# Performance work log

Measured on AMD Instinct MI355X. Metric: run time of the kernel, lower is better.

## Reference

```python
import jax, jax.numpy as jnp
import numpy as np

NUM_ITER = 5
DIM = 512
BATCH = 64


def setup_inputs() -> dict:
    key = jax.random.key(0)
    a = jax.random.normal(key, (BATCH, DIM, DIM), dtype=jnp.float32)
    # Symmetric PSD input (covariance-like), as in bilinear pooling; Newton-Schulz
    # requires SPD matrices for convergence.
    x = jnp.einsum('bik,bjk->bij', a, a) / DIM
    I = jnp.eye(DIM, dtype=jnp.float32)
    return {"x": x, "I": I}


def reference(x, I):
    # x: [bs, dim, dim]; I: [dim, dim]
    normA = jnp.sqrt(jnp.sum(x * x, axis=(1, 2), keepdims=True))  # Frobenius norm per matrix
    Y = x / normA
    bs, dim, _ = x.shape
    Z = jnp.broadcast_to(I, (bs, dim, dim))
    Ib = Z
    for _ in range(NUM_ITER):
        T = 0.5 * (3.0 * Ib - jnp.matmul(Z, Y))
        Y = jnp.matmul(Y, T)
        Z = jnp.matmul(T, Z)
    sA = Y * jnp.sqrt(normA)
    return sA
```

## Files before the change

kernel.cpp:

```cpp
#include <hip/hip_runtime.h>
#include <hip/hip_bf16.h>
#include <stdint.h>

#define DIM   512
#define BATCH 64
#define KENC  1024
#define BM    256
#define BN    256
#define BKT   32
#define NKT   16
#define BUFE  32768

typedef __attribute__((ext_vector_type(8))) short short8;
typedef __attribute__((ext_vector_type(4))) float floatx4;

__device__ __forceinline__ ushort f2bf(float f) {
    __hip_bfloat16 h = __float2bfloat16(f);
    return *(ushort*)&h;
}
__device__ __forceinline__ float bf2f(ushort u) {
    __hip_bfloat16 h = *(__hip_bfloat16*)&u;
    return (float)h;
}

typedef __attribute__((address_space(3))) uint32_t lds_u32;
typedef const __attribute__((address_space(1))) uint32_t glb_u32;
__device__ __forceinline__ void gload16(const ushort* g, ushort* l) {
    __builtin_amdgcn_global_load_lds((glb_u32*)g, (lds_u32*)l, 16, 0, 0);
}

#define WAITVM(N) asm volatile("s_waitcnt vmcnt(" #N ")" ::: "memory")
#define BARRIER() do { __builtin_amdgcn_s_barrier(); __builtin_amdgcn_sched_barrier(0); } while (0)

__global__ __launch_bounds__(256) void norm_partial_kernel(const float* __restrict__ x,
                                                           float* __restrict__ partial) {
    int b = blockIdx.y;
    int i = blockIdx.x;
    const float4* xv = (const float4*)(x + (size_t)b * DIM * DIM + (size_t)i * (DIM * DIM / 16));
    float s = 0.f;
    #pragma unroll
    for (int r = 0; r < 16; ++r) {
        float4 v = xv[r * 256 + threadIdx.x];
        s += v.x * v.x + v.y * v.y + v.z * v.z + v.w * v.w;
    }
    #pragma unroll
    for (int off = 32; off > 0; off >>= 1) s += __shfl_down(s, off, 64);
    __shared__ float red[4];
    int lane = threadIdx.x & 63, wid = threadIdx.x >> 6;
    if (lane == 0) red[wid] = s;
    __syncthreads();
    if (threadIdx.x == 0) partial[b * 16 + i] = red[0] + red[1] + red[2] + red[3];
}

__global__ __launch_bounds__(256) void init_kernel(const float* __restrict__ x,
                                                   const float* __restrict__ partial,
                                                   float* __restrict__ norms,
                                                   ushort* __restrict__ Yenc,
                                                   ushort* __restrict__ Tenc) {
    int b = blockIdx.y;
    float s = 0.f;
    #pragma unroll
    for (int p = 0; p < 16; ++p) s += partial[b * 16 + p];
    float nrm = sqrtf(s);
    if (blockIdx.x == 0 && threadIdx.x == 0) norms[b] = nrm;
    float inv = 1.0f / nrm;
    int idx = (blockIdx.x * 256 + threadIdx.x) * 4;
    int r = idx >> 9;
    int c = idx & 511;
    float4 v = *(const float4*)(x + (size_t)b * DIM * DIM + idx);
    float yv[4] = {v.x * inv, v.y * inv, v.z * inv, v.w * inv};
    size_t base = (size_t)b * DIM * KENC + (size_t)r * KENC;
    ushort yhi[4], ylo[4], thi[4], tlo[4];
    #pragma unroll
    for (int j = 0; j < 4; ++j) {
        float y = yv[j];
        yhi[j] = f2bf(y);
        ylo[j] = f2bf(y - bf2f(yhi[j]));
        float t = ((c + j) == r ? 1.5f : 0.0f) - 0.5f * y;
        thi[j] = f2bf(t);
        tlo[j] = f2bf(t - bf2f(thi[j]));
    }
    *(ushort4*)(Yenc + base + c)       = *(ushort4*)yhi;
    *(ushort4*)(Yenc + base + 512 + c) = *(ushort4*)ylo;
    *(ushort4*)(Tenc + base + c)       = *(ushort4*)thi;
    *(ushort4*)(Tenc + base + 512 + c) = *(ushort4*)tlo;
}

__device__ __forceinline__ void stage_hi(ushort* buf, const ushort* Ag, const ushort* Bg,
                                         int k0, int tid) {
    #pragma unroll
    for (int s = 0; s < 2; ++s) {
        int vt = tid + s * 512;
        int row = vt >> 2;
        int pc  = vt & 3;
        int kc  = ((pc ^ ((row >> 1) & 3)) << 3);
        const ushort* ar = Ag + (size_t)row * KENC + k0 + kc;
        const ushort* br = Bg + (size_t)row * KENC + k0 + kc;
        gload16(ar, &buf[vt * 8]);
        gload16(br, &buf[16384 + vt * 8]);
    }
}
__device__ __forceinline__ void stage_lo(ushort* buf, const ushort* Ag, const ushort* Bg,
                                         int k0, int tid) {
    #pragma unroll
    for (int s = 0; s < 2; ++s) {
        int vt = tid + s * 512;
        int row = vt >> 2;
        int pc  = vt & 3;
        int kc  = ((pc ^ ((row >> 1) & 3)) << 3);
        const ushort* ar = Ag + (size_t)row * KENC + k0 + kc;
        const ushort* br = Bg + (size_t)row * KENC + k0 + kc;
        gload16(ar + 512, &buf[8192 + vt * 8]);
        gload16(br + 512, &buf[24576 + vt * 8]);
    }
}

__device__ __forceinline__ void store_enc(ushort* Cenc, size_t matoff, int gr, int gc, float v) {
    ushort hi = f2bf(v);
    ushort lo = f2bf(v - bf2f(hi));
    Cenc[matoff + (size_t)gr * KENC + gc] = hi;
    Cenc[matoff + (size_t)gr * KENC + 512 + gc] = lo;
}

template <int MODE>
__global__ __launch_bounds__(512, 2) void gemm_bt(const ushort* __restrict__ A,
                                                  const ushort* __restrict__ B,
                                                  ushort* __restrict__ Cenc,
                                                  float* __restrict__ Cout,
                                                  const float* __restrict__ norms) {
    __shared__ __attribute__((aligned(16))) ushort sm[2 * BUFE];

    int f = blockIdx.x;
    int xcd = f & 7;
    int g   = f >> 3;
    int b   = xcd + 8 * (g >> 2);
    int t   = g & 3;
    int bm  = t >> 1;
    int bn  = t & 1;

    size_t matoff = (size_t)b * DIM * KENC;
    const ushort* Ag = A + matoff + (size_t)bm * BM * KENC;
    const ushort* Bg = B + matoff + (size_t)bn * BN * KENC;

    int tid = threadIdx.x;
    int wave = tid >> 6, lane = tid & 63;
    int lane15 = lane & 15, quad = lane >> 4;
    int wrow = (wave >> 2) * 128;
    int wcol = (wave & 3) * 64;
    int s2 = (lane15 >> 1) & 3;
    int fo = ((quad ^ s2) << 3);

    floatx4 acc[8][4];
    #pragma unroll
    for (int i = 0; i < 8; ++i)
        #pragma unroll
        for (int j = 0; j < 4; ++j)
            acc[i][j] = (floatx4){0.f, 0.f, 0.f, 0.f};

    stage_hi(sm, Ag, Bg, 0, tid);
    stage_lo(sm, Ag, Bg, 0, tid);
    WAITVM(4);
    BARRIER();

    short8 ah[8], bh[4], bl[4], al[8];
    #pragma unroll
    for (int i = 0; i < 8; ++i)
        ah[i] = *(const short8*)&sm[(wrow + i * 16 + lane15) * BKT + fo];
    #pragma unroll
    for (int j = 0; j < 4; ++j)
        bh[j] = *(const short8*)&sm[16384 + (wcol + j * 16 + lane15) * BKT + fo];

    for (int kt = 0; kt < NKT; ++kt) {
        const ushort* cur = sm + (kt & 1) * BUFE;
        ushort* nxt = sm + ((kt + 1) & 1) * BUFE;
        const ushort* Asl = cur + 8192;
        const ushort* Bsl = cur + 24576;

        if (kt + 1 < NKT) stage_hi(nxt, Ag, Bg, (kt + 1) * BKT, tid);
        __builtin_amdgcn_s_setprio(1);
        #pragma unroll
        for (int i = 0; i < 8; ++i)
            #pragma unroll
            for (int j = 0; j < 4; ++j)
                acc[i][j] = __builtin_amdgcn_mfma_f32_16x16x32_bf16(ah[i], bh[j], acc[i][j], 0, 0, 0);
        __builtin_amdgcn_s_setprio(0);

        if (kt + 1 < NKT) { WAITVM(4); } else { WAITVM(0); }
        BARRIER();

        #pragma unroll
        for (int j = 0; j < 4; ++j)
            bl[j] = *(const short8*)&Bsl[(wcol + j * 16 + lane15) * BKT + fo];
        #pragma unroll
        for (int i = 0; i < 8; ++i)
            al[i] = *(const short8*)&Asl[(wrow + i * 16 + lane15) * BKT + fo];
        if (kt + 1 < NKT) stage_lo(nxt, Ag, Bg, (kt + 1) * BKT, tid);
        __builtin_amdgcn_s_setprio(1);
        #pragma unroll
        for (int i = 0; i < 8; ++i)
            #pragma unroll
            for (int j = 0; j < 4; ++j)
                acc[i][j] = __builtin_amdgcn_mfma_f32_16x16x32_bf16(ah[i], bl[j], acc[i][j], 0, 0, 0);
        #pragma unroll
        for (int i = 0; i < 8; ++i)
            #pragma unroll
            for (int j = 0; j < 4; ++j)
                acc[i][j] = __builtin_amdgcn_mfma_f32_16x16x32_bf16(al[i], bh[j], acc[i][j], 0, 0, 0);
        __builtin_amdgcn_s_setprio(0);

        if (kt + 1 < NKT) {
            WAITVM(4);
            BARRIER();
            #pragma unroll
            for (int i = 0; i < 8; ++i)
                ah[i] = *(const short8*)&nxt[(wrow + i * 16 + lane15) * BKT + fo];
            #pragma unroll
            for (int j = 0; j < 4; ++j)
                bh[j] = *(const short8*)&nxt[16384 + (wcol + j * 16 + lane15) * BKT + fo];
        }
    }

    float scale = (MODE == 2) ? sqrtf(norms[b]) : 0.f;
    #pragma unroll
    for (int i = 0; i < 8; ++i) {
        int gr0 = bm * BM + wrow + i * 16 + quad * 4;
        #pragma unroll
        for (int j = 0; j < 4; ++j) {
            int gc = bn * BN + wcol + j * 16 + lane15;
            #pragma unroll
            for (int rr = 0; rr < 4; ++rr) {
                int gr = gr0 + rr;
                float cv = acc[i][j][rr];
                if (MODE == 0) {
                    store_enc(Cenc, matoff, gr, gc, (gr == gc ? 1.5f : 0.0f) - 0.5f * cv);
                } else if (MODE == 1) {
                    store_enc(Cenc, matoff, gr, gc, cv);
                } else {
                    Cout[(size_t)b * DIM * DIM + (size_t)gr * DIM + gc] = cv * scale;
                }
            }
        }
    }
}

extern "C" void kernel_launch(void* const* d_in, const int* in_sizes, int n_in,
                              void* d_out, int out_size, void* d_ws, size_t ws_size,
                              hipStream_t stream) {
    const float* x = (const float*)d_in[0];
    float* out = (float*)d_out;

    const size_t MATB = (size_t)BATCH * DIM * KENC * sizeof(ushort);
    char* ws = (char*)d_ws;
    ushort* W0 = (ushort*)(ws + 0 * MATB);
    ushort* W1 = (ushort*)(ws + 1 * MATB);
    ushort* W2 = (ushort*)(ws + 2 * MATB);
    float* partial = (float*)(ws + 3 * MATB);
    float* norms   = (float*)(ws + 3 * MATB + 4096);
    ushort* D = (ushort*)d_out;

    dim3 gblk(512);
    dim3 g1(256);

    norm_partial_kernel<<<dim3(16, BATCH), 256, 0, stream>>>(x, partial);
    init_kernel<<<dim3(256, BATCH), 256, 0, stream>>>(x, partial, norms, W0, W1);

    gemm_bt<1><<<g1, gblk, 0, stream>>>(W0, W1, W2, nullptr, nullptr);
    gemm_bt<0><<<g1, gblk, 0, stream>>>(W1, W2, W0, nullptr, nullptr);
    gemm_bt<1><<<g1, gblk, 0, stream>>>(W2, W0, D, nullptr, nullptr);
    gemm_bt<1><<<g1, gblk, 0, stream>>>(W0, W1, W2, nullptr, nullptr);
    gemm_bt<0><<<g1, gblk, 0, stream>>>(W2, D, W0, nullptr, nullptr);
    gemm_bt<1><<<g1, gblk, 0, stream>>>(D, W0, W1, nullptr, nullptr);
    gemm_bt<1><<<g1, gblk, 0, stream>>>(W0, W2, D, nullptr, nullptr);
    gemm_bt<0><<<g1, gblk, 0, stream>>>(D, W1, W0, nullptr, nullptr);
    gemm_bt<1><<<g1, gblk, 0, stream>>>(W1, W0, W2, nullptr, nullptr);
    gemm_bt<1><<<g1, gblk, 0, stream>>>(W0, D, W1, nullptr, nullptr);
    gemm_bt<0><<<g1, gblk, 0, stream>>>(W1, W2, W0, nullptr, nullptr);
    gemm_bt<2><<<g1, gblk, 0, stream>>>(W2, W0, nullptr, out, norms);
}
```

Before: 725.8 us.

## Interleave hi/lo bf16 split encoding and stage full tile per k-step

Changes the split-bf16 encoding from separate hi and lo half-rows to interleaved hi/lo pairs, so init and epilogue write one packed 32-bit or 128-bit store per element instead of two scattered 16-bit stores. The GEMM now stages the whole interleaved tile in one pass with a new XOR swizzle and de-interleaves fragments in registers with byte permutes. This replaces the two-phase hi/lo pipeline with a single wait and barrier per k-step. It cuts store transactions and barrier count, but adds permute ALU work and a full vmcnt(0) wait at each step, which may expose load latency.

```diff
diff --git a/kernel.cpp b/kernel.cpp
--- a/kernel.cpp
+++ b/kernel.cpp
@@ -70,56 +70,50 @@
     float4 v = *(const float4*)(x + (size_t)b * DIM * DIM + idx);
     float yv[4] = {v.x * inv, v.y * inv, v.z * inv, v.w * inv};
     size_t base = (size_t)b * DIM * KENC + (size_t)r * KENC;
-    ushort yhi[4], ylo[4], thi[4], tlo[4];
+    ushort yp[8], tp[8];
     #pragma unroll
     for (int j = 0; j < 4; ++j) {
         float y = yv[j];
-        yhi[j] = f2bf(y);
-        ylo[j] = f2bf(y - bf2f(yhi[j]));
+        ushort yh = f2bf(y);
+        yp[2 * j]     = yh;
+        yp[2 * j + 1] = f2bf(y - bf2f(yh));
         float t = ((c + j) == r ? 1.5f : 0.0f) - 0.5f * y;
-        thi[j] = f2bf(t);
-        tlo[j] = f2bf(t - bf2f(thi[j]));
-    }
-    *(ushort4*)(Yenc + base + c)       = *(ushort4*)yhi;
-    *(ushort4*)(Yenc + base + 512 + c) = *(ushort4*)ylo;
-    *(ushort4*)(Tenc + base + c)       = *(ushort4*)thi;
-    *(ushort4*)(Tenc + base + 512 + c) = *(ushort4*)tlo;
-}
-
-__device__ __forceinline__ void stage_hi(ushort* buf, const ushort* Ag, const ushort* Bg,
-                                         int k0, int tid) {
-    #pragma unroll
-    for (int s = 0; s < 2; ++s) {
-        int vt = tid + s * 512;
-        int row = vt >> 2;
-        int pc  = vt & 3;
-        int kc  = ((pc ^ ((row >> 1) & 3)) << 3);
-        const ushort* ar = Ag + (size_t)row * KENC + k0 + kc;
-        const ushort* br = Bg + (size_t)row * KENC + k0 + kc;
-        gload16(ar, &buf[vt * 8]);
-        gload16(br, &buf[16384 + vt * 8]);
-    }
-}
-__device__ __forceinline__ void stage_lo(ushort* buf, const ushort* Ag, const ushort* Bg,
-                                         int k0, int tid) {
-    #pragma unroll
-    for (int s = 0; s < 2; ++s) {
-        int vt = tid + s * 512;
-        int row = vt >> 2;
-        int pc  = vt & 3;
-        int kc  = ((pc ^ ((row >> 1) & 3)) << 3);
-        const ushort* ar = Ag + (size_t)row * KENC + k0 + kc;
-        const ushort* br = Bg + (size_t)row * KENC + k0 + kc;
-        gload16(ar + 512, &buf[8192 + vt * 8]);
-        gload16(br + 512, &buf[24576 + vt * 8]);
-    }
-}
-
-__device__ __forceinline__ void store_enc(ushort* Cenc, size_t matoff, int gr, int gc, float v) {
-    ushort hi = f2bf(v);
-    ushort lo = f2bf(v - bf2f(hi));
-    Cenc[matoff + (size_t)gr * KENC + gc] = hi;
-    Cenc[matoff + (size_t)gr * KENC + 512 + gc] = lo;
+        ushort th = f2bf(t);
+        tp[2 * j]     = th;
+        tp[2 * j + 1] = f2bf(t - bf2f(th));
+    }
+    *(short8*)(Yenc + base + 2 * c) = *(short8*)yp;
+    *(short8*)(Tenc + base + 2 * c) = *(short8*)tp;
+}
+
+__device__ __forceinline__ void stage_tile(ushort* buf, const ushort* Ag, const ushort* Bg,
+                                           int k0, int tid) {
+    #pragma unroll
+    for (int s = 0; s < 4; ++s) {
+        int vt  = tid + s * 512;
+        int row = vt >> 3;
+        int pc  = vt & 7;
+        int kc  = pc ^ (row & 7);
+        size_t go = (size_t)row * KENC + 2 * k0 + kc * 8;
+        gload16(Ag + go, &buf[vt * 8]);
+        gload16(Bg + go, &buf[16384 + vt * 8]);
+    }
+}
+
+__device__ __forceinline__ uint32_t prm(uint32_t hi, uint32_t lo, uint32_t sel) {
+    return __builtin_amdgcn_perm(hi, lo, sel);
+}
+__device__ __forceinline__ void rdpair(const ushort* rowbase, int q, int r7,
+                                       short8& h, short8& l) {
+    const uint4 u0 = *(const uint4*)(rowbase + (((2 * q)     ^ r7) << 3));
+    const uint4 u1 = *(const uint4*)(rowbase + (((2 * q + 1) ^ r7) << 3));
+    uint4 rh, rl;
+    rh.x = prm(u0.y, u0.x, 0x05040100u); rh.y = prm(u0.w, u0.z, 0x05040100u);
+    rh.z = prm(u1.y, u1.x, 0x05040100u); rh.w = prm(u1.w, u1.z, 0x05040100u);
+    rl.x = prm(u0.y, u0.x, 0x07060302u); rl.y = prm(u0.w, u0.z, 0x07060302u);
+    rl.z = prm(u1.y, u1.x, 0x07060302u); rl.w = prm(u1.w, u1.z, 0x07060302u);
+    h = *(short8*)&rh;
+    l = *(short8*)&rl;
 }
 
 template <int MODE>
@@ -147,8 +141,7 @@
     int lane15 = lane & 15, quad = lane >> 4;
     int wrow = (wave >> 2) * 128;
     int wcol = (wave & 3) * 64;
-    int s2 = (lane15 >> 1) & 3;
-    int fo = ((quad ^ s2) << 3);
+    int r7 = lane15 & 7;
 
     floatx4 acc[8][4];
     #pragma unroll
@@ -157,45 +150,32 @@
         for (int j = 0; j < 4; ++j)
             acc[i][j] = (floatx4){0.f, 0.f, 0.f, 0.f};
 
-    stage_hi(sm, Ag, Bg, 0, tid);
-    stage_lo(sm, Ag, Bg, 0, tid);
-    WAITVM(4);
-    BARRIER();
-
-    short8 ah[8], bh[4], bl[4], al[8];
-    #pragma unroll
-    for (int i = 0; i < 8; ++i)
-        ah[i] = *(const short8*)&sm[(wrow + i * 16 + lane15) * BKT + fo];
-    #pragma unroll
-    for (int j = 0; j < 4; ++j)
-        bh[j] = *(const short8*)&sm[16384 + (wcol + j * 16 + lane15) * BKT + fo];
+    stage_tile(sm, Ag, Bg, 0, tid);
 
     for (int kt = 0; kt < NKT; ++kt) {
+        WAITVM(0);
+        BARRIER();
         const ushort* cur = sm + (kt & 1) * BUFE;
         ushort* nxt = sm + ((kt + 1) & 1) * BUFE;
-        const ushort* Asl = cur + 8192;
-        const ushort* Bsl = cur + 24576;
-
-        if (kt + 1 < NKT) stage_hi(nxt, Ag, Bg, (kt + 1) * BKT, tid);
+        const ushort* Abase = cur;
+        const ushort* Bbase = cur + 16384;
+
+        short8 ah[8], al[8], bh[4], bl[4];
+        #pragma unroll
+        for (int i = 0; i < 8; ++i)
+            rdpair(&Abase[(wrow + i * 16 + lane15) * 64], quad, r7, ah[i], al[i]);
+        #pragma unroll
+        for (int j = 0; j < 4; ++j)
+            rdpair(&Bbase[(wcol + j * 16 + lane15) * 64], quad, r7, bh[j], bl[j]);
+
+        if (kt + 1 < NKT) stage_tile(nxt, Ag, Bg, (kt + 1) * BKT, tid);
+
         __builtin_amdgcn_s_setprio(1);
         #pragma unroll
         for (int i = 0; i < 8; ++i)
             #pragma unroll
             for (int j = 0; j < 4; ++j)
                 acc[i][j] = __builtin_amdgcn_mfma_f32_16x16x32_bf16(ah[i], bh[j], acc[i][j], 0, 0, 0);
-        __builtin_amdgcn_s_setprio(0);
-
-        if (kt + 1 < NKT) { WAITVM(4); } else { WAITVM(0); }
-        BARRIER();
-
-        #pragma unroll
-        for (int j = 0; j < 4; ++j)
-            bl[j] = *(const short8*)&Bsl[(wcol + j * 16 + lane15) * BKT + fo];
-        #pragma unroll
-        for (int i = 0; i < 8; ++i)
-            al[i] = *(const short8*)&Asl[(wrow + i * 16 + lane15) * BKT + fo];
-        if (kt + 1 < NKT) stage_lo(nxt, Ag, Bg, (kt + 1) * BKT, tid);
-        __builtin_amdgcn_s_setprio(1);
         #pragma unroll
         for (int i = 0; i < 8; ++i)
             #pragma unroll
@@ -207,17 +187,6 @@
             for (int j = 0; j < 4; ++j)
                 acc[i][j] = __builtin_amdgcn_mfma_f32_16x16x32_bf16(al[i], bh[j], acc[i][j], 0, 0, 0);
         __builtin_amdgcn_s_setprio(0);
-
-        if (kt + 1 < NKT) {
-            WAITVM(4);
-            BARRIER();
-            #pragma unroll
-            for (int i = 0; i < 8; ++i)
-                ah[i] = *(const short8*)&nxt[(wrow + i * 16 + lane15) * BKT + fo];
-            #pragma unroll
-            for (int j = 0; j < 4; ++j)
-                bh[j] = *(const short8*)&nxt[16384 + (wcol + j * 16 + lane15) * BKT + fo];
-        }
     }
 
     float scale = (MODE == 2) ? sqrtf(norms[b]) : 0.f;
@@ -231,12 +200,14 @@
             for (int rr = 0; rr < 4; ++rr) {
                 int gr = gr0 + rr;
                 float cv = acc[i][j][rr];
-                if (MODE == 0) {
-                    store_enc(Cenc, matoff, gr, gc, (gr == gc ? 1.5f : 0.0f) - 0.5f * cv);
-                } else if (MODE == 1) {
-                    store_enc(Cenc, matoff, gr, gc, cv);
+                if (MODE == 2) {
+                    Cout[(size_t)b * DIM * DIM + (size_t)gr * DIM + gc] = cv * scale;
                 } else {
-                    Cout[(size_t)b * DIM * DIM + (size_t)gr * DIM + gc] = cv * scale;
+                    float v = (MODE == 0) ? ((gr == gc ? 1.5f : 0.0f) - 0.5f * cv) : cv;
+                    ushort hi = f2bf(v);
+                    ushort lo = f2bf(v - bf2f(hi));
+                    *(uint32_t*)&Cenc[matoff + (size_t)gr * KENC + 2 * gc] =
+                        (uint32_t)hi | ((uint32_t)lo << 16);
                 }
             }
         }
```

New measurement: 772.8 us. 6.5% more time.
